# Performance work log

Hardware: AMD Instinct MI355X
Metric: run time of the kernel (lower is better)

The kernel has to match this reference:

```python
import jax, jax.numpy as jnp
import numpy as np

B, S, D, H = 2, 2048, 1024, 16
HD = D // H  # head_dim = 64


def setup_inputs() -> dict:
    key = jax.random.key(0)
    ks = jax.random.split(key, 6)
    scale = D ** -0.5
    x = jax.random.normal(ks[0], (B, S, D), dtype=jnp.float32)
    wq = jax.random.normal(ks[1], (D, D), dtype=jnp.float32) * scale
    wk = jax.random.normal(ks[2], (D, D), dtype=jnp.float32) * scale
    wv = jax.random.normal(ks[3], (D, D), dtype=jnp.float32) * scale
    wo = jax.random.normal(ks[4], (D, D), dtype=jnp.float32) * scale
    # RoPE frequencies: theta_i = 10000^(-2i/HD), angles[t, i] = t * theta_i
    inv_freq = 1.0 / (10000.0 ** (np.arange(0, HD, 2, dtype=np.float32) / HD))
    t = np.arange(S, dtype=np.float32)
    angles = np.outer(t, inv_freq)  # [S, HD//2]
    freqs_cos = jnp.asarray(np.cos(angles), dtype=jnp.float32)
    freqs_sin = jnp.asarray(np.sin(angles), dtype=jnp.float32)
    # additive causal mask [1,1,S,S]
    neg = jnp.float32(-1e9)
    mask = jnp.triu(jnp.full((S, S), neg, dtype=jnp.float32), k=1)[None, None]
    return {"x": x, "wq": wq, "wk": wk, "wv": wv, "wo": wo,
            "freqs_cos": freqs_cos, "freqs_sin": freqs_sin,
            "mask": mask, "start_pos": 0}


def _apply_rope(q, freqs_cos, freqs_sin):
    # q: [B, S, H, HD] -> pairs (even, odd) rotated by angle per position
    b, s, h, hd = q.shape
    q2 = q.reshape(b, s, h, hd // 2, 2)
    qr, qi = q2[..., 0], q2[..., 1]
    c = freqs_cos[None, :, None, :]  # [1, S, 1, HD//2]
    sn = freqs_sin[None, :, None, :]
    out_r = qr * c - qi * sn
    out_i = qr * sn + qi * c
    return jnp.stack([out_r, out_i], axis=-1).reshape(b, s, h, hd)


def reference(x, wq, wk, wv, wo, freqs_cos, freqs_sin, mask, start_pos):
    b, s, _ = x.shape
    xq = (x @ wq).reshape(b, s, H, HD)
    xk = (x @ wk).reshape(b, s, H, HD)
    xv = (x @ wv).reshape(b, s, H, HD)
    xq = _apply_rope(xq, freqs_cos, freqs_sin)
    xk = _apply_rope(xk, freqs_cos, freqs_sin)
    # [B, H, S, HD]
    q = xq.transpose(0, 2, 1, 3)
    k = xk.transpose(0, 2, 1, 3)
    v = xv.transpose(0, 2, 1, 3)
    scores = jnp.einsum('bhqd,bhkd->bhqk', q, k) / jnp.sqrt(jnp.float32(HD))
    scores = scores + mask
    probs = jax.nn.softmax(scores.astype(jnp.float32), axis=-1).astype(q.dtype)
    out = jnp.einsum('bhqk,bhkd->bhqd', probs, v)
    out = out.transpose(0, 2, 1, 3).reshape(b, s, H * HD)
    return out @ wo
```

## Files before the change

kernel.cpp:

```cpp
#include <hip/hip_runtime.h>

typedef unsigned short u16;
typedef __bf16 bf16x8 __attribute__((ext_vector_type(8)));
typedef float f32x4 __attribute__((ext_vector_type(4)));

#define DD 1024
#define SS 2048
#define HH 16
#define HDIM 64

__device__ __forceinline__ u16 f2bf(float f) {
  union { float f; unsigned u; } x; x.f = f;
  unsigned r = x.u + 0x7FFFu + ((x.u >> 16) & 1u);
  return (u16)(r >> 16);
}

__device__ __forceinline__ u16 f2bf_s(float f) {
  unsigned r;
  asm("v_cvt_pk_bf16_f32 %0, %1, %2" : "=v"(r) : "v"(f), "v"(0.f));
  return (u16)r;
}

__device__ __forceinline__ void gload_lds16(const u16* g, u16* l) {
  __builtin_amdgcn_global_load_lds((const __attribute__((address_space(1))) void*)g,
                                   (__attribute__((address_space(3))) void*)l, 16, 0, 0);
}

__global__ __launch_bounds__(256) void cvt_x(const float* __restrict__ in, u16* __restrict__ out, int n) {
  int i = (blockIdx.x * 256 + threadIdx.x) * 4;
  if (i + 3 < n) {
    float4 v = *(const float4*)(in + i);
    out[i + 0] = f2bf(v.x);
    out[i + 1] = f2bf(v.y);
    out[i + 2] = f2bf(v.z);
    out[i + 3] = f2bf(v.w);
  }
}

__global__ __launch_bounds__(256) void transpose_w(const float* __restrict__ w0, const float* __restrict__ w1,
                                                   const float* __restrict__ w2, const float* __restrict__ w3,
                                                   u16* __restrict__ out) {
  __shared__ float t[32][33];
  const float* w = (blockIdx.z == 0) ? w0 : (blockIdx.z == 1) ? w1 : (blockIdx.z == 2) ? w2 : w3;
  u16* o = out + (size_t)blockIdx.z * DD * DD;
  int j0 = blockIdx.x * 32;
  int i0 = blockIdx.y * 32;
  int tx = threadIdx.x, ty = threadIdx.y;
#pragma unroll
  for (int r = ty; r < 32; r += 8)
    t[r][tx] = w[(size_t)(i0 + r) * DD + j0 + tx];
  __syncthreads();
#pragma unroll
  for (int r = ty; r < 32; r += 8)
    o[(size_t)(j0 + r) * DD + i0 + tx] = f2bf(t[tx][r]);
}

__device__ __forceinline__ void gemm_128(const u16* __restrict__ A, const u16* __restrict__ BT,
                                         int m0, int n0, int K, u16* As, u16* Bs, f32x4 acc[4][4]) {
  const int tid = threadIdx.x;
  const int lane = tid & 63;
  const int wid = tid >> 6;
  const int wm = wid >> 1, wn = wid & 1;
  const int lr = lane & 15;
  const int lg = lane >> 4;
#pragma unroll
  for (int i = 0; i < 4; ++i)
#pragma unroll
    for (int j = 0; j < 4; ++j)
      acc[i][j] = (f32x4){0.f, 0.f, 0.f, 0.f};

  for (int kt = 0; kt < K / 64; ++kt) {
    int k0 = kt * 64;
    __syncthreads();
#pragma unroll
    for (int i = 0; i < 4; ++i) {
      int c = i * 256 + tid;
      int row = c >> 3;
      int j = (c & 7) ^ (row & 7);
      gload_lds16(A + (size_t)(m0 + row) * K + k0 + j * 8, As + c * 8);
      gload_lds16(BT + (size_t)(n0 + row) * K + k0 + j * 8, Bs + c * 8);
    }
    __syncthreads();
#pragma unroll
    for (int ks = 0; ks < 2; ++ks) {
      bf16x8 af[4], bfr[4];
#pragma unroll
      for (int mi = 0; mi < 4; ++mi) {
        int row = wm * 64 + mi * 16 + lr;
        int ch = (ks * 4 + lg) ^ (row & 7);
        af[mi] = *(const bf16x8*)(As + row * 64 + ch * 8);
      }
#pragma unroll
      for (int ni = 0; ni < 4; ++ni) {
        int row = wn * 64 + ni * 16 + lr;
        int ch = (ks * 4 + lg) ^ (row & 7);
        bfr[ni] = *(const bf16x8*)(Bs + row * 64 + ch * 8);
      }
      __builtin_amdgcn_s_setprio(1);
#pragma unroll
      for (int mi = 0; mi < 4; ++mi)
#pragma unroll
        for (int ni = 0; ni < 4; ++ni)
          acc[mi][ni] = __builtin_amdgcn_mfma_f32_16x16x32_bf16(af[mi], bfr[ni], acc[mi][ni], 0, 0, 0);
      __builtin_amdgcn_s_setprio(0);
    }
  }
}

__global__ __launch_bounds__(256, 2) void gemm_qkv(const u16* __restrict__ xb, const u16* __restrict__ wT,
                                                   const float* __restrict__ fc, const float* __restrict__ fs,
                                                   u16* __restrict__ Qr, u16* __restrict__ Kr, u16* __restrict__ Vt) {
  __shared__ u16 As[128 * 64], Bs[128 * 64];
  const int z = blockIdx.z;
  const u16* BT = wT + (size_t)z * DD * DD;
  f32x4 acc[4][4];
  int m0 = blockIdx.x * 128, n0 = blockIdx.y * 128;
  gemm_128(xb, BT, m0, n0, DD, As, Bs, acc);

  const int lane = threadIdx.x & 63, wid = threadIdx.x >> 6;
  const int wm = wid >> 1, wn = wid & 1, lr = lane & 15, lg = lane >> 4;
#pragma unroll
  for (int mi = 0; mi < 4; ++mi)
#pragma unroll
    for (int ni = 0; ni < 4; ++ni)
#pragma unroll
      for (int j = 0; j < 4; ++j) {
        int m = m0 + wm * 64 + mi * 16 + lg * 4 + j;
        int n = n0 + wn * 64 + ni * 16 + lr;
        float v = acc[mi][ni][j];
        int b = m >> 11, s = m & 2047;
        int h = n >> 6, hd = n & 63;
        if (z == 2) {
          Vt[((size_t)(b * HH + h) * HDIM + hd) * SS + s] = f2bf(v);
        } else {
          float pv = __shfl_xor(v, 1);
          int fi = s * 32 + (hd >> 1);
          float c = fc[fi], sn = fs[fi];
          float o = ((hd & 1) == 0) ? (v * c - pv * sn) : (pv * sn + v * c);
          u16* dst = (z == 0) ? Qr : Kr;
          dst[((size_t)(b * HH + h) * SS + s) * HDIM + hd] = f2bf(o);
        }
      }
}

__device__ __forceinline__ void stage_tile(const u16* __restrict__ Kh, const u16* __restrict__ Vh,
                                           int i2, u16* Kbuf, u16* Vbuf, int tid) {
#pragma unroll
  for (int k = 0; k < 2; ++k) {
    const int c = tid + k * 512;
    const int tt = c >> 9, cl = c & 511;
    const int row = cl >> 3, j = (cl & 7) ^ (row & 7);
    gload_lds16(Kh + (size_t)(i2 * 128 + tt * 64 + row) * HDIM + j * 8, Kbuf + c * 8);
    gload_lds16(Vh + (size_t)row * SS + i2 * 128 + tt * 64 + j * 8, Vbuf + c * 8);
  }
}

__device__ __forceinline__ void attn_pass(int qt, int bh, const u16* __restrict__ Qh,
                                          const u16* __restrict__ Kh, const u16* __restrict__ Vh,
                                          u16* __restrict__ Ob, u16* KbR, u16* VbR, u16* Pw,
                                          int gid, int wq) {
  const int tid = threadIdx.x;
  const int lane = tid & 63;
  const int lr = lane & 15, lg = lane >> 4;
  const int q0 = qt * 64 + wq * 16;

  bf16x8 aq[2];
#pragma unroll
  for (int ks = 0; ks < 2; ++ks)
    aq[ks] = *(const bf16x8*)(Qh + (q0 + lr) * HDIM + ks * 32 + lg * 8);

  bf16x8 ones;
  {
    union { u16 u[8]; bf16x8 v; } ou;
#pragma unroll
    for (int i = 0; i < 8; ++i) ou.u[i] = 0x3F80;
    ones = ou.v;
  }

  f32x4 o[4];
#pragma unroll
  for (int d = 0; d < 4; ++d) o[d] = (f32x4){0.f, 0.f, 0.f, 0.f};
  f32x4 ls = (f32x4){0.f, 0.f, 0.f, 0.f};

  const int n2 = (qt + 2) >> 1;

  __syncthreads();
  stage_tile(Kh, Vh, 0, KbR, VbR, tid);

  for (int i = 0; i < n2; ++i) {
    const int cur = i & 1;
    __syncthreads();
    if (i + 1 < n2) stage_tile(Kh, Vh, i + 1, KbR + (cur ^ 1) * 8192, VbR + (cur ^ 1) * 8192, tid);

    const int t = 2 * i + gid;
    const u16* Kt = KbR + cur * 8192 + gid * 4096;
    const u16* Vtl = VbR + cur * 8192 + gid * 4096;

    f32x4 sc[4];
#pragma unroll
    for (int kb = 0; kb < 4; ++kb) sc[kb] = (f32x4){0.f, 0.f, 0.f, 0.f};
    __builtin_amdgcn_s_setprio(1);
#pragma unroll
    for (int ks = 0; ks < 2; ++ks)
#pragma unroll
      for (int kb = 0; kb < 4; ++kb) {
        int row = kb * 16 + lr;
        int ch = (ks * 4 + lg) ^ (row & 7);
        bf16x8 bk = *(const bf16x8*)(Kt + row * 64 + ch * 8);
        sc[kb] = __builtin_amdgcn_mfma_f32_16x16x32_bf16(aq[ks], bk, sc[kb], 0, 0, 0);
      }
    __builtin_amdgcn_s_setprio(0);

    if (t >= qt) {
#pragma unroll
      for (int kb = 0; kb < 4; ++kb)
#pragma unroll
        for (int j = 0; j < 4; ++j) {
          int q = q0 + lg * 4 + j;
          int kk = t * 64 + kb * 16 + lr;
          float e = __expf(sc[kb][j] * 0.125f);
          sc[kb][j] = (kk > q) ? 0.f : e;
        }
    } else {
#pragma unroll
      for (int kb = 0; kb < 4; ++kb)
#pragma unroll
        for (int j = 0; j < 4; ++j)
          sc[kb][j] = __expf(sc[kb][j] * 0.125f);
    }

#pragma unroll
    for (int kb = 0; kb < 4; ++kb)
#pragma unroll
      for (int j = 0; j < 4; ++j) {
        int rr = lg * 4 + j;
        int ccol = kb * 16 + lr;
        int ch = (ccol >> 3) ^ (rr & 7);
        Pw[rr * 64 + ch * 8 + (ccol & 7)] = f2bf_s(sc[kb][j]);
      }
#pragma unroll
    for (int ks = 0; ks < 2; ++ks) {
      int chp = (ks * 4 + lg) ^ (lr & 7);
      bf16x8 ap = *(const bf16x8*)(Pw + lr * 64 + chp * 8);
      __builtin_amdgcn_s_setprio(1);
      ls = __builtin_amdgcn_mfma_f32_16x16x32_bf16(ap, ones, ls, 0, 0, 0);
#pragma unroll
      for (int d = 0; d < 4; ++d) {
        int row = d * 16 + lr;
        int ch = (ks * 4 + lg) ^ (row & 7);
        bf16x8 bv = *(const bf16x8*)(Vtl + row * 64 + ch * 8);
        o[d] = __builtin_amdgcn_mfma_f32_16x16x32_bf16(ap, bv, o[d], 0, 0, 0);
      }
      __builtin_amdgcn_s_setprio(0);
    }
  }

  __syncthreads();
  float* mo = (float*)KbR;
  float* ml = (float*)VbR;
  if (gid == 1) {
#pragma unroll
    for (int d = 0; d < 4; ++d)
#pragma unroll
      for (int j = 0; j < 4; ++j)
        mo[(wq * 16 + lg * 4 + j) * 64 + d * 16 + lr] = o[d][j];
    if (lr == 0) {
#pragma unroll
      for (int j = 0; j < 4; ++j) ml[wq * 16 + lg * 4 + j] = ls[j];
    }
  }
  __syncthreads();
  if (gid == 0) {
    const int b = bh >> 4, h = bh & 15;
#pragma unroll
    for (int j = 0; j < 4; ++j) ls[j] += ml[wq * 16 + lg * 4 + j];
#pragma unroll
    for (int d = 0; d < 4; ++d)
#pragma unroll
      for (int j = 0; j < 4; ++j) {
        float val = o[d][j] + mo[(wq * 16 + lg * 4 + j) * 64 + d * 16 + lr];
        int s = q0 + lg * 4 + j;
        int col = h * HDIM + d * 16 + lr;
        Ob[((size_t)b * SS + s) * DD + col] = f2bf(val / ls[j]);
      }
  }
}

__global__ __launch_bounds__(512, 4) void attn(const u16* __restrict__ Qr, const u16* __restrict__ Kr,
                                               const u16* __restrict__ Vt, u16* __restrict__ Ob) {
  __shared__ u16 Kb[2][2][64 * 64];
  __shared__ u16 Vb[2][2][64 * 64];
  __shared__ u16 Ps[8][16 * 64];
  const int id = blockIdx.x;
  const int xcd = id & 7;
  const int r = id >> 3;
  const int pair = r & 15;
  const int bh = xcd * 4 + (r >> 4);
  const u16* Qh = Qr + (size_t)bh * SS * HDIM;
  const u16* Kh = Kr + (size_t)bh * SS * HDIM;
  const u16* Vh = Vt + (size_t)bh * HDIM * SS;
  const int wid = threadIdx.x >> 6;
  const int gid = wid >> 2, wq = wid & 3;
  u16* Pw = &Ps[wid][0];
  attn_pass(pair, bh, Qh, Kh, Vh, Ob, &Kb[0][0][0], &Vb[0][0][0], Pw, gid, wq);
  attn_pass(31 - pair, bh, Qh, Kh, Vh, Ob, &Kb[0][0][0], &Vb[0][0][0], Pw, gid, wq);
}

__global__ __launch_bounds__(256, 2) void gemm_wo(const u16* __restrict__ Ab, const u16* __restrict__ woT,
                                                  float* __restrict__ out) {
  __shared__ u16 As[128 * 64], Bs[128 * 64];
  f32x4 acc[4][4];
  int m0 = blockIdx.x * 128, n0 = blockIdx.y * 128;
  gemm_128(Ab, woT, m0, n0, DD, As, Bs, acc);
  const int lane = threadIdx.x & 63, wid = threadIdx.x >> 6;
  const int wm = wid >> 1, wn = wid & 1, lr = lane & 15, lg = lane >> 4;
#pragma unroll
  for (int mi = 0; mi < 4; ++mi)
#pragma unroll
    for (int ni = 0; ni < 4; ++ni)
#pragma unroll
      for (int j = 0; j < 4; ++j) {
        int m = m0 + wm * 64 + mi * 16 + lg * 4 + j;
        int n = n0 + wn * 64 + ni * 16 + lr;
        out[(size_t)m * DD + n] = acc[mi][ni][j];
      }
}

extern "C" void kernel_launch(void* const* d_in, const int* in_sizes, int n_in,
                              void* d_out, int out_size, void* d_ws, size_t ws_size,
                              hipStream_t stream) {
  const float* x  = (const float*)d_in[0];
  const float* wq = (const float*)d_in[1];
  const float* wk = (const float*)d_in[2];
  const float* wv = (const float*)d_in[3];
  const float* wo = (const float*)d_in[4];
  const float* fc = (const float*)d_in[5];
  const float* fs = (const float*)d_in[6];
  float* out = (float*)d_out;

  char* ws = (char*)d_ws;
  u16* xb = (u16*)(ws);
  u16* wT = (u16*)(ws + (8ull << 20));
  u16* Qr = (u16*)(ws + (16ull << 20));
  u16* Kr = (u16*)(ws + (24ull << 20));
  u16* Vt = (u16*)(ws + (32ull << 20));
  u16* Ob = (u16*)(ws + (40ull << 20));

  cvt_x<<<4096, 256, 0, stream>>>(x, xb, 4096 * 1024);
  transpose_w<<<dim3(32, 32, 4), dim3(32, 8), 0, stream>>>(wq, wk, wv, wo, wT);
  gemm_qkv<<<dim3(32, 8, 3), 256, 0, stream>>>(xb, wT, fc, fs, Qr, Kr, Vt);
  attn<<<512, 512, 0, stream>>>(Qr, Kr, Vt, Ob);
  gemm_wo<<<dim3(32, 8), 256, 0, stream>>>(Ob, wT + 3ull * DD * DD, out);
}
```

Before: 120.0 us.

## Double-buffer GEMM LDS tiles and fuse QKV into one 128x192 tiled launch

Both GEMMs now double-buffer their LDS tiles, so the next K-slice loads while MFMAs run on the current one, and one barrier per iteration replaces two. The QKV GEMM treats the three weight matrices as a single concatenated N=3072 matrix. It uses 512-thread blocks over 128x192 tiles (a 32x16 grid instead of 32x8x3) and works out q/k/v per 16-column fragment. The cost is twice the LDS per block, which may lower occupancy, and the 48-column warp split may leave the MFMA issue pattern less balanced.

```diff
diff --git a/kernel.cpp b/kernel.cpp
--- a/kernel.cpp
+++ b/kernel.cpp
@@ -55,81 +55,81 @@
     o[(size_t)(j0 + r) * DD + i0 + tx] = f2bf(t[tx][r]);
 }
 
-__device__ __forceinline__ void gemm_128(const u16* __restrict__ A, const u16* __restrict__ BT,
-                                         int m0, int n0, int K, u16* As, u16* Bs, f32x4 acc[4][4]) {
+__global__ __launch_bounds__(512, 4) void gemm_qkv(const u16* __restrict__ xb, const u16* __restrict__ wT,
+                                                   const float* __restrict__ fc, const float* __restrict__ fs,
+                                                   u16* __restrict__ Qr, u16* __restrict__ Kr, u16* __restrict__ Vt) {
+  __shared__ u16 As[2][128 * 64];
+  __shared__ u16 Bs[2][192 * 64];
   const int tid = threadIdx.x;
-  const int lane = tid & 63;
-  const int wid = tid >> 6;
-  const int wm = wid >> 1, wn = wid & 1;
-  const int lr = lane & 15;
-  const int lg = lane >> 4;
+  const int lane = tid & 63, wid = tid >> 6;
+  const int wm = wid >> 2, wn = wid & 3;
+  const int lr = lane & 15, lg = lane >> 4;
+  const int m0 = blockIdx.x * 128, n0 = blockIdx.y * 192;
+
+  f32x4 acc[4][3];
 #pragma unroll
   for (int i = 0; i < 4; ++i)
 #pragma unroll
-    for (int j = 0; j < 4; ++j)
-      acc[i][j] = (f32x4){0.f, 0.f, 0.f, 0.f};
-
-  for (int kt = 0; kt < K / 64; ++kt) {
-    int k0 = kt * 64;
+    for (int j = 0; j < 3; ++j) acc[i][j] = (f32x4){0.f, 0.f, 0.f, 0.f};
+
+  auto stage = [&](int buf, int k0) {
+#pragma unroll
+    for (int i = 0; i < 2; ++i) {
+      int c = tid + i * 512;
+      int row = c >> 3, j = (c & 7) ^ (row & 7);
+      gload_lds16(xb + (size_t)(m0 + row) * DD + k0 + j * 8, &As[buf][c * 8]);
+    }
+#pragma unroll
+    for (int i = 0; i < 3; ++i) {
+      int c = tid + i * 512;
+      int row = c >> 3, j = (c & 7) ^ (row & 7);
+      gload_lds16(wT + (size_t)(n0 + row) * DD + k0 + j * 8, &Bs[buf][c * 8]);
+    }
+  };
+
+  stage(0, 0);
+  for (int kt = 0; kt < 16; ++kt) {
+    const int cur = kt & 1;
     __syncthreads();
-#pragma unroll
-    for (int i = 0; i < 4; ++i) {
-      int c = i * 256 + tid;
-      int row = c >> 3;
-      int j = (c & 7) ^ (row & 7);
-      gload_lds16(A + (size_t)(m0 + row) * K + k0 + j * 8, As + c * 8);
-      gload_lds16(BT + (size_t)(n0 + row) * K + k0 + j * 8, Bs + c * 8);
-    }
-    __syncthreads();
+    if (kt < 15) stage(cur ^ 1, (kt + 1) * 64);
 #pragma unroll
     for (int ks = 0; ks < 2; ++ks) {
-      bf16x8 af[4], bfr[4];
+      bf16x8 af[4], bfr[3];
 #pragma unroll
       for (int mi = 0; mi < 4; ++mi) {
         int row = wm * 64 + mi * 16 + lr;
         int ch = (ks * 4 + lg) ^ (row & 7);
-        af[mi] = *(const bf16x8*)(As + row * 64 + ch * 8);
-      }
-#pragma unroll
-      for (int ni = 0; ni < 4; ++ni) {
-        int row = wn * 64 + ni * 16 + lr;
-        int ch = (ks * 4 + lg) ^ (row & 7);
-        bfr[ni] = *(const bf16x8*)(Bs + row * 64 + ch * 8);
+        af[mi] = *(const bf16x8*)(&As[cur][row * 64 + ch * 8]);
+      }
+#pragma unroll
+      for (int ni = 0; ni < 3; ++ni) {
+        int row = wn * 48 + ni * 16 + lr;
+        int ch = (ks * 4 + lg) ^ (row & 7);
+        bfr[ni] = *(const bf16x8*)(&Bs[cur][row * 64 + ch * 8]);
       }
       __builtin_amdgcn_s_setprio(1);
 #pragma unroll
       for (int mi = 0; mi < 4; ++mi)
 #pragma unroll
-        for (int ni = 0; ni < 4; ++ni)
+        for (int ni = 0; ni < 3; ++ni)
           acc[mi][ni] = __builtin_amdgcn_mfma_f32_16x16x32_bf16(af[mi], bfr[ni], acc[mi][ni], 0, 0, 0);
       __builtin_amdgcn_s_setprio(0);
     }
   }
-}
-
-__global__ __launch_bounds__(256, 2) void gemm_qkv(const u16* __restrict__ xb, const u16* __restrict__ wT,
-                                                   const float* __restrict__ fc, const float* __restrict__ fs,
-                                                   u16* __restrict__ Qr, u16* __restrict__ Kr, u16* __restrict__ Vt) {
-  __shared__ u16 As[128 * 64], Bs[128 * 64];
-  const int z = blockIdx.z;
-  const u16* BT = wT + (size_t)z * DD * DD;
-  f32x4 acc[4][4];
-  int m0 = blockIdx.x * 128, n0 = blockIdx.y * 128;
-  gemm_128(xb, BT, m0, n0, DD, As, Bs, acc);
-
-  const int lane = threadIdx.x & 63, wid = threadIdx.x >> 6;
-  const int wm = wid >> 1, wn = wid & 1, lr = lane & 15, lg = lane >> 4;
+
 #pragma unroll
   for (int mi = 0; mi < 4; ++mi)
 #pragma unroll
-    for (int ni = 0; ni < 4; ++ni)
+    for (int ni = 0; ni < 3; ++ni) {
+      const int nb = n0 + wn * 48 + ni * 16;
+      const int z = nb >> 10;
+      const int nn = (nb & 1023) + lr;
+      const int h = nn >> 6, hd = nn & 63;
 #pragma unroll
       for (int j = 0; j < 4; ++j) {
         int m = m0 + wm * 64 + mi * 16 + lg * 4 + j;
-        int n = n0 + wn * 64 + ni * 16 + lr;
         float v = acc[mi][ni][j];
         int b = m >> 11, s = m & 2047;
-        int h = n >> 6, hd = n & 63;
         if (z == 2) {
           Vt[((size_t)(b * HH + h) * HDIM + hd) * SS + s] = f2bf(v);
         } else {
@@ -141,6 +141,7 @@
           dst[((size_t)(b * HH + h) * SS + s) * HDIM + hd] = f2bf(o);
         }
       }
+    }
 }
 
 __device__ __forceinline__ void stage_tile(const u16* __restrict__ Kh, const u16* __restrict__ Vh,
@@ -308,12 +309,62 @@
 
 __global__ __launch_bounds__(256, 2) void gemm_wo(const u16* __restrict__ Ab, const u16* __restrict__ woT,
                                                   float* __restrict__ out) {
-  __shared__ u16 As[128 * 64], Bs[128 * 64];
+  __shared__ u16 As[2][128 * 64];
+  __shared__ u16 Bs[2][128 * 64];
+  const int tid = threadIdx.x;
+  const int lane = tid & 63, wid = tid >> 6;
+  const int wm = wid >> 1, wn = wid & 1;
+  const int lr = lane & 15, lg = lane >> 4;
+  const int m0 = blockIdx.x * 128, n0 = blockIdx.y * 128;
+
   f32x4 acc[4][4];
-  int m0 = blockIdx.x * 128, n0 = blockIdx.y * 128;
-  gemm_128(Ab, woT, m0, n0, DD, As, Bs, acc);
-  const int lane = threadIdx.x & 63, wid = threadIdx.x >> 6;
-  const int wm = wid >> 1, wn = wid & 1, lr = lane & 15, lg = lane >> 4;
+#pragma unroll
+  for (int i = 0; i < 4; ++i)
+#pragma unroll
+    for (int j = 0; j < 4; ++j) acc[i][j] = (f32x4){0.f, 0.f, 0.f, 0.f};
+
+  auto stage = [&](int buf, int k0) {
+#pragma unroll
+    for (int i = 0; i < 4; ++i) {
+      int c = i * 256 + tid;
+      int row = c >> 3, j = (c & 7) ^ (row & 7);
+      gload_lds16(Ab + (size_t)(m0 + row) * DD + k0 + j * 8, &As[buf][c * 8]);
+      gload_lds16(woT + (size_t)(n0 + row) * DD + k0 + j * 8, &Bs[buf][c * 8]);
+    }
+  };
+
+  stage(0, 0);
+  for (int kt = 0; kt < 16; ++kt) {
+    const int cur = kt & 1;
+    __syncthreads();
+    if (kt < 15) stage(cur ^ 1, (kt + 1) * 64);
+#pragma unroll
+    for (int ks = 0; ks < 2; ++ks) {
+      bf16x8 af[4], bfr[4];
+#pragma unroll
+      for (int mi = 0; mi < 4; ++mi) {
+        int row = wm * 64 + mi * 16 + lr;
+        int ch = (ks * 4 + lg) ^ (row & 7);
+        af[mi] = *(const bf16x8*)(&As[cur][row * 64 + ch * 8]);
+      }
+#pragma unroll
+      for (int ni = 0; ni < 4; ++ni) {
+        int row = wn * 64 + ni * 16 + lr;
+        int ch = (ks * 4 + lg) ^ (row & 7);
+        bfr[ni] = *(const bf16x8*)(&Bs[cur][row * 64 + ch * 8]);
+      }
+      __builtin_amdgcn_s_setprio(1);
+#pragma unroll
+      for (int mi = 0; mi < 4; ++mi)
+#pragma unroll
+        for (int ni = 0; ni < 4; ++ni)
+          acc[mi][ni] = __builtin_amdgcn_mfma_f32_16x16x32_bf16(af[mi], bfr[ni], acc[mi][ni], 0, 0, 0);
+      __builtin_amdgcn_s_setprio(0);
+    }
+  }
+
+  const int lane2 = threadIdx.x & 63;
+  (void)lane2;
 #pragma unroll
   for (int mi = 0; mi < 4; ++mi)
 #pragma unroll
@@ -348,7 +399,7 @@
 
   cvt_x<<<4096, 256, 0, stream>>>(x, xb, 4096 * 1024);
   transpose_w<<<dim3(32, 32, 4), dim3(32, 8), 0, stream>>>(wq, wk, wv, wo, wT);
-  gemm_qkv<<<dim3(32, 8, 3), 256, 0, stream>>>(xb, wT, fc, fs, Qr, Kr, Vt);
+  gemm_qkv<<<dim3(32, 16), 512, 0, stream>>>(xb, wT, fc, fs, Qr, Kr, Vt);
   attn<<<512, 512, 0, stream>>>(Qr, Kr, Vt, Ob);
   gemm_wo<<<dim3(32, 8), 256, 0, stream>>>(Ob, wT + 3ull * DD * DD, out);
 }
```

After: 118.6 us. Within noise of the previous version (-1.1%).
